# Kernel optimization log

Measured on AMD Instinct MI355X. Metric: run time of the kernel, lower is better.

The kernel has to match this reference:

```python
import jax, jax.numpy as jnp
import numpy as np

# Fuzzy-logic decoder: rules = [[0,0,0],[1,0,1]] (hardcoded in the torch module's __init__).
# For each rule [p, a, b] firing on predicate p:
#   num[s,o] = max_k min(t[a, s, k], t[b, k, o])   (max-min relation composition)
# amalgamate(x, y) = x + y - x*y (probabilistic OR); new starts at 0, and
# amalgamate(x, 0) = x, so with exactly one rule per predicate:
#   t_new[p] = amalgamate(t[p], num_p) = t[p] + num_p - t[p]*num_p

def _compose(A, B):
    # A: [S, K], B: [K, O] -> max over k of elementwise min -> [S, O]
    return jnp.max(jnp.minimum(A[:, :, None], B[None, :, :]), axis=1)


def setup_inputs() -> dict:
    key = jax.random.key(0)
    t = jax.random.uniform(key, (2, 512, 512), dtype=jnp.float32)
    return {"t": t}


def reference(t) -> jnp.ndarray:
    t0, t1 = t[0], t[1]
    num0 = _compose(t0, t0)          # rule [0,0,0]
    num1 = _compose(t0, t1)          # rule [1,0,1]
    num = jnp.stack([num0, num1], axis=0)  # [2, S, O]
    return t + num - t * num         # amalgamate(t, num)
```

## Files before the change

### kernel.cpp

```cpp
#include <hip/hip_runtime.h>


#define SDIM 512
#define TS 64
#define TO 32
#define BK 64
#define BK2 32
#define NCH (SDIM / BK)
#define ASTR 36

typedef _Float16 h2 __attribute__((ext_vector_type(2)));

__device__ __forceinline__ h2 pack2(float a, float b) {
    return __builtin_bit_cast(h2, __builtin_amdgcn_cvt_pkrtz(a, b));
}
__device__ __forceinline__ h2 pmin(h2 a, h2 b) { return __builtin_elementwise_min(a, b); }
__device__ __forceinline__ h2 pmax(h2 a, h2 b) { return __builtin_elementwise_max(a, b); }

__global__ __launch_bounds__(256) void fuzzy_compose_kernel(
        const float* __restrict__ t, float* __restrict__ out) {
    __shared__ h2 Als[TS][ASTR];
    __shared__ h2 Bls[BK2][TO];

    const int tid = threadIdx.x;
    const int o0 = blockIdx.x * TO;
    const int s0 = blockIdx.y * TS;
    const int p  = blockIdx.z;

    const float* __restrict__ A = t;
    const float* __restrict__ B = t + p * (SDIM * SDIM);

    const int og = tid & 15, sg = tid >> 4;
    const int ol = og * 2, sl = sg * 4;

    const int ar = tid >> 2, aq = tid & 3;
    const int bk = tid >> 3, bq = tid & 7;

    const float4* __restrict__ Arow =
        reinterpret_cast<const float4*>(A + (s0 + ar) * SDIM);

    h2 acc[4][2];
    #pragma unroll
    for (int j = 0; j < 4; ++j)
        #pragma unroll
        for (int i = 0; i < 2; ++i)
            acc[j][i] = pack2(0.f, 0.f);

    float4 fa[4], fx, fy;
    #pragma unroll
    for (int q4 = 0; q4 < 4; ++q4) fa[q4] = Arow[aq * 4 + q4];
    fx = *reinterpret_cast<const float4*>(B + (2 * bk) * SDIM + o0 + bq * 4);
    fy = *reinterpret_cast<const float4*>(B + (2 * bk + 1) * SDIM + o0 + bq * 4);

    for (int c = 0; c < NCH; ++c) {
        #pragma unroll
        for (int q4 = 0; q4 < 4; ++q4) {
            Als[ar][aq * 8 + q4 * 2 + 0] = pack2(fa[q4].x, fa[q4].y);
            Als[ar][aq * 8 + q4 * 2 + 1] = pack2(fa[q4].z, fa[q4].w);
        }
        Bls[bk][bq * 4 + 0] = pack2(fx.x, fy.x);
        Bls[bk][bq * 4 + 1] = pack2(fx.y, fy.y);
        Bls[bk][bq * 4 + 2] = pack2(fx.z, fy.z);
        Bls[bk][bq * 4 + 3] = pack2(fx.w, fy.w);
        __syncthreads();

        if (c + 1 < NCH) {
            const int k0 = (c + 1) * BK;
            #pragma unroll
            for (int q4 = 0; q4 < 4; ++q4) fa[q4] = Arow[k0 / 4 + aq * 4 + q4];
            fx = *reinterpret_cast<const float4*>(B + (k0 + 2 * bk) * SDIM + o0 + bq * 4);
            fy = *reinterpret_cast<const float4*>(B + (k0 + 2 * bk + 1) * SDIM + o0 + bq * 4);
        }

        #pragma unroll
        for (int k2 = 0; k2 < BK2; ++k2) {
            const h2 b0 = Bls[k2][ol];
            const h2 b1 = Bls[k2][ol + 1];
            #pragma unroll
            for (int j = 0; j < 4; ++j) {
                const h2 a = Als[sl + j][k2];
                acc[j][0] = pmax(acc[j][0], pmin(a, b0));
                acc[j][1] = pmax(acc[j][1], pmin(a, b1));
            }
        }
        __syncthreads();
    }

    const float* __restrict__ tp = t + p * (SDIM * SDIM);
    float* __restrict__ op = out + p * (SDIM * SDIM);
    #pragma unroll
    for (int j = 0; j < 4; ++j) {
        const int row = s0 + sl + j;
        const float2 tv = *reinterpret_cast<const float2*>(tp + row * SDIM + o0 + ol);
        const float n0 = fmaxf((float)acc[j][0][0], (float)acc[j][0][1]);
        const float n1 = fmaxf((float)acc[j][1][0], (float)acc[j][1][1]);
        float2 r;
        r.x = tv.x + n0 - tv.x * n0;
        r.y = tv.y + n1 - tv.y * n1;
        *reinterpret_cast<float2*>(op + row * SDIM + o0 + ol) = r;
    }
}

extern "C" void kernel_launch(void* const* d_in, const int* in_sizes, int n_in,
                              void* d_out, int out_size, void* d_ws, size_t ws_size,
                              hipStream_t stream) {
    const float* t = (const float*)d_in[0];
    float* out = (float*)d_out;
    dim3 grid(SDIM / TO, SDIM / TS, 2);
    fuzzy_compose_kernel<<<grid, 256, 0, stream>>>(t, out);
}
```

Measured before the change: 72.22 us.

## Split K across blocks with fp16 partials and a max-reduce finalize kernel

Measured after the change: 139.0 us. 1.92x slower.

```diff
diff --git a/kernel.cpp b/kernel.cpp
--- a/kernel.cpp
+++ b/kernel.cpp
@@ -4,10 +4,11 @@
 #define SDIM 512
 #define TS 64
 #define TO 32
+#define SPLIT 4
+#define KB 128
 #define BK 64
 #define BK2 32
-#define NCH (SDIM / BK)
-#define ASTR 36
+#define NCH (KB / BK)
 
 typedef _Float16 h2 __attribute__((ext_vector_type(2)));
 
@@ -16,89 +17,117 @@
 }
 __device__ __forceinline__ h2 pmin(h2 a, h2 b) { return __builtin_elementwise_min(a, b); }
 __device__ __forceinline__ h2 pmax(h2 a, h2 b) { return __builtin_elementwise_max(a, b); }
+__device__ __forceinline__ h2 bch2(unsigned u) { return __builtin_bit_cast(h2, u); }
 
-__global__ __launch_bounds__(256) void fuzzy_compose_kernel(
-        const float* __restrict__ t, float* __restrict__ out) {
-    __shared__ h2 Als[TS][ASTR];
+__global__ __launch_bounds__(256, 4) void compose_part(
+        const float* __restrict__ t, _Float16* __restrict__ part) {
+    __shared__ h2 AlsT[BK2][TS];
     __shared__ h2 Bls[BK2][TO];
 
     const int tid = threadIdx.x;
     const int o0 = blockIdx.x * TO;
     const int s0 = blockIdx.y * TS;
-    const int p  = blockIdx.z;
+    const int p  = blockIdx.z >> 2;
+    const int sp = blockIdx.z & 3;
+    const int kbase = sp * KB;
 
-    const float* __restrict__ A = t;
     const float* __restrict__ B = t + p * (SDIM * SDIM);
 
-    const int og = tid & 15, sg = tid >> 4;
-    const int ol = og * 2, sl = sg * 4;
-
+    const int ol = (tid & 15) * 2, sl = (tid >> 4) * 4;
     const int ar = tid >> 2, aq = tid & 3;
     const int bk = tid >> 3, bq = tid & 7;
 
     const float4* __restrict__ Arow =
-        reinterpret_cast<const float4*>(A + (s0 + ar) * SDIM);
+        reinterpret_cast<const float4*>(t + (s0 + ar) * SDIM + kbase);
 
     h2 acc[4][2];
     #pragma unroll
-    for (int j = 0; j < 4; ++j)
-        #pragma unroll
-        for (int i = 0; i < 2; ++i)
-            acc[j][i] = pack2(0.f, 0.f);
+    for (int j = 0; j < 4; ++j) {
+        acc[j][0] = pack2(0.f, 0.f);
+        acc[j][1] = pack2(0.f, 0.f);
+    }
 
     float4 fa[4], fx, fy;
     #pragma unroll
     for (int q4 = 0; q4 < 4; ++q4) fa[q4] = Arow[aq * 4 + q4];
-    fx = *reinterpret_cast<const float4*>(B + (2 * bk) * SDIM + o0 + bq * 4);
-    fy = *reinterpret_cast<const float4*>(B + (2 * bk + 1) * SDIM + o0 + bq * 4);
+    fx = *reinterpret_cast<const float4*>(B + (kbase + 2 * bk) * SDIM + o0 + bq * 4);
+    fy = *reinterpret_cast<const float4*>(B + (kbase + 2 * bk + 1) * SDIM + o0 + bq * 4);
 
+    #pragma unroll
     for (int c = 0; c < NCH; ++c) {
         #pragma unroll
         for (int q4 = 0; q4 < 4; ++q4) {
-            Als[ar][aq * 8 + q4 * 2 + 0] = pack2(fa[q4].x, fa[q4].y);
-            Als[ar][aq * 8 + q4 * 2 + 1] = pack2(fa[q4].z, fa[q4].w);
+            const int k2 = aq * 8 + q4 * 2;
+            AlsT[k2 + 0][ar] = pack2(fa[q4].x, fa[q4].y);
+            AlsT[k2 + 1][ar] = pack2(fa[q4].z, fa[q4].w);
         }
-        Bls[bk][bq * 4 + 0] = pack2(fx.x, fy.x);
-        Bls[bk][bq * 4 + 1] = pack2(fx.y, fy.y);
-        Bls[bk][bq * 4 + 2] = pack2(fx.z, fy.z);
-        Bls[bk][bq * 4 + 3] = pack2(fx.w, fy.w);
+        {
+            h2 b0 = pack2(fx.x, fy.x), b1 = pack2(fx.y, fy.y);
+            h2 b2 = pack2(fx.z, fy.z), b3 = pack2(fx.w, fy.w);
+            uint4 u;
+            u.x = __builtin_bit_cast(unsigned, b0);
+            u.y = __builtin_bit_cast(unsigned, b1);
+            u.z = __builtin_bit_cast(unsigned, b2);
+            u.w = __builtin_bit_cast(unsigned, b3);
+            *reinterpret_cast<uint4*>(&Bls[bk][bq * 4]) = u;
+        }
         __syncthreads();
 
         if (c + 1 < NCH) {
             const int k0 = (c + 1) * BK;
             #pragma unroll
             for (int q4 = 0; q4 < 4; ++q4) fa[q4] = Arow[k0 / 4 + aq * 4 + q4];
-            fx = *reinterpret_cast<const float4*>(B + (k0 + 2 * bk) * SDIM + o0 + bq * 4);
-            fy = *reinterpret_cast<const float4*>(B + (k0 + 2 * bk + 1) * SDIM + o0 + bq * 4);
+            fx = *reinterpret_cast<const float4*>(B + (kbase + k0 + 2 * bk) * SDIM + o0 + bq * 4);
+            fy = *reinterpret_cast<const float4*>(B + (kbase + k0 + 2 * bk + 1) * SDIM + o0 + bq * 4);
         }
 
         #pragma unroll
         for (int k2 = 0; k2 < BK2; ++k2) {
-            const h2 b0 = Bls[k2][ol];
-            const h2 b1 = Bls[k2][ol + 1];
-            #pragma unroll
-            for (int j = 0; j < 4; ++j) {
-                const h2 a = Als[sl + j][k2];
-                acc[j][0] = pmax(acc[j][0], pmin(a, b0));
-                acc[j][1] = pmax(acc[j][1], pmin(a, b1));
-            }
+            const uint4 ua = *reinterpret_cast<const uint4*>(&AlsT[k2][sl]);
+            const uint2 ub = *reinterpret_cast<const uint2*>(&Bls[k2][ol]);
+            const h2 b0 = bch2(ub.x), b1 = bch2(ub.y);
+            const h2 a0 = bch2(ua.x), a1 = bch2(ua.y), a2 = bch2(ua.z), a3 = bch2(ua.w);
+            acc[0][0] = pmax(acc[0][0], pmin(a0, b0));
+            acc[0][1] = pmax(acc[0][1], pmin(a0, b1));
+            acc[1][0] = pmax(acc[1][0], pmin(a1, b0));
+            acc[1][1] = pmax(acc[1][1], pmin(a1, b1));
+            acc[2][0] = pmax(acc[2][0], pmin(a2, b0));
+            acc[2][1] = pmax(acc[2][1], pmin(a2, b1));
+            acc[3][0] = pmax(acc[3][0], pmin(a3, b0));
+            acc[3][1] = pmax(acc[3][1], pmin(a3, b1));
         }
         __syncthreads();
     }
 
-    const float* __restrict__ tp = t + p * (SDIM * SDIM);
-    float* __restrict__ op = out + p * (SDIM * SDIM);
     #pragma unroll
     for (int j = 0; j < 4; ++j) {
-        const int row = s0 + sl + j;
-        const float2 tv = *reinterpret_cast<const float2*>(tp + row * SDIM + o0 + ol);
         const float n0 = fmaxf((float)acc[j][0][0], (float)acc[j][0][1]);
         const float n1 = fmaxf((float)acc[j][1][0], (float)acc[j][1][1]);
-        float2 r;
-        r.x = tv.x + n0 - tv.x * n0;
-        r.y = tv.y + n1 - tv.y * n1;
-        *reinterpret_cast<float2*>(op + row * SDIM + o0 + ol) = r;
+        const h2 pr = pack2(n0, n1);
+        const int idx = ((p * SPLIT + sp) * SDIM + (s0 + sl + j)) * SDIM + o0 + ol;
+        *reinterpret_cast<h2*>(part + idx) = pr;
     }
+}
+
+__global__ __launch_bounds__(256) void finalize_kernel(
+        const float* __restrict__ t, const _Float16* __restrict__ part,
+        float* __restrict__ out) {
+    const int i2 = blockIdx.x * 256 + threadIdx.x;
+    const h2* __restrict__ ph = reinterpret_cast<const h2*>(part);
+    const int ps = i2 >> 8;
+    const int c2 = i2 & 255;
+    const int p = ps >> 9, s = ps & 511;
+    const int base = (p * SPLIT) * (SDIM * SDIM / 2) + s * (SDIM / 2) + c2;
+    h2 m = ph[base];
+    m = pmax(m, ph[base + 1 * (SDIM * SDIM / 2)]);
+    m = pmax(m, ph[base + 2 * (SDIM * SDIM / 2)]);
+    m = pmax(m, ph[base + 3 * (SDIM * SDIM / 2)]);
+    const float2 tv = reinterpret_cast<const float2*>(t)[i2];
+    const float n0 = (float)m[0], n1 = (float)m[1];
+    float2 r;
+    r.x = tv.x + n0 - tv.x * n0;
+    r.y = tv.y + n1 - tv.y * n1;
+    reinterpret_cast<float2*>(out)[i2] = r;
 }
 
 extern "C" void kernel_launch(void* const* d_in, const int* in_sizes, int n_in,
@@ -106,6 +135,11 @@
                               hipStream_t stream) {
     const float* t = (const float*)d_in[0];
     float* out = (float*)d_out;
-    dim3 grid(SDIM / TO, SDIM / TS, 2);
-    fuzzy_compose_kernel<<<grid, 256, 0, stream>>>(t, out);
+    _Float16* part = (_Float16*)d_ws;
+
+    dim3 grid1(SDIM / TO, SDIM / TS, 2 * SPLIT);
+    compose_part<<<grid1, 256, 0, stream>>>(t, part);
+
+    const int n2 = 2 * SDIM * SDIM / 2;
+    finalize_kernel<<<n2 / 256, 256, 0, stream>>>(t, part, out);
 }
```

## Halve row tile, transpose and swizzle A in LDS, vectorize LDS reads

Applied to the files above, without the earlier changes.

New measurement: 69.55 us. 1.04x faster.

```diff
diff --git a/kernel.cpp b/kernel.cpp
--- a/kernel.cpp
+++ b/kernel.cpp
@@ -2,12 +2,12 @@
 
 
 #define SDIM 512
-#define TS 64
+#define TS 32
 #define TO 32
 #define BK 64
 #define BK2 32
 #define NCH (SDIM / BK)
-#define ASTR 36
+#define BSTR 36
 
 typedef _Float16 h2 __attribute__((ext_vector_type(2)));
 
@@ -16,72 +16,73 @@
 }
 __device__ __forceinline__ h2 pmin(h2 a, h2 b) { return __builtin_elementwise_min(a, b); }
 __device__ __forceinline__ h2 pmax(h2 a, h2 b) { return __builtin_elementwise_max(a, b); }
+__device__ __forceinline__ h2 bch2(unsigned u) { return __builtin_bit_cast(h2, u); }
 
-__global__ __launch_bounds__(256) void fuzzy_compose_kernel(
+__global__ __launch_bounds__(256, 2) void fuzzy_compose_kernel(
         const float* __restrict__ t, float* __restrict__ out) {
-    __shared__ h2 Als[TS][ASTR];
-    __shared__ h2 Bls[BK2][TO];
+    __shared__ h2 AlsT[BK2][TS];
+    __shared__ h2 Bls[BK2][BSTR];
 
     const int tid = threadIdx.x;
     const int o0 = blockIdx.x * TO;
     const int s0 = blockIdx.y * TS;
     const int p  = blockIdx.z;
 
-    const float* __restrict__ A = t;
     const float* __restrict__ B = t + p * (SDIM * SDIM);
 
-    const int og = tid & 15, sg = tid >> 4;
-    const int ol = og * 2, sl = sg * 4;
-
-    const int ar = tid >> 2, aq = tid & 3;
-    const int bk = tid >> 3, bq = tid & 7;
+    const int ol = (tid & 15) * 2, sl = (tid >> 4) * 2;
+    const int ar = tid >> 3, aq = tid & 7;
+    const int acol = ar ^ (aq << 2);
+    const int bk2 = tid >> 3, bq = tid & 7;
 
     const float4* __restrict__ Arow =
-        reinterpret_cast<const float4*>(A + (s0 + ar) * SDIM);
+        reinterpret_cast<const float4*>(t + (s0 + ar) * SDIM);
 
-    h2 acc[4][2];
-    #pragma unroll
-    for (int j = 0; j < 4; ++j)
-        #pragma unroll
-        for (int i = 0; i < 2; ++i)
-            acc[j][i] = pack2(0.f, 0.f);
+    h2 acc[2][2];
+    acc[0][0] = pack2(0.f, 0.f); acc[0][1] = pack2(0.f, 0.f);
+    acc[1][0] = pack2(0.f, 0.f); acc[1][1] = pack2(0.f, 0.f);
 
-    float4 fa[4], fx, fy;
-    #pragma unroll
-    for (int q4 = 0; q4 < 4; ++q4) fa[q4] = Arow[aq * 4 + q4];
-    fx = *reinterpret_cast<const float4*>(B + (2 * bk) * SDIM + o0 + bq * 4);
-    fy = *reinterpret_cast<const float4*>(B + (2 * bk + 1) * SDIM + o0 + bq * 4);
+    float4 fa0, fa1, fx, fy;
+    fa0 = Arow[aq * 2 + 0];
+    fa1 = Arow[aq * 2 + 1];
+    fx = *reinterpret_cast<const float4*>(B + (2 * bk2) * SDIM + o0 + bq * 4);
+    fy = *reinterpret_cast<const float4*>(B + (2 * bk2 + 1) * SDIM + o0 + bq * 4);
 
     for (int c = 0; c < NCH; ++c) {
-        #pragma unroll
-        for (int q4 = 0; q4 < 4; ++q4) {
-            Als[ar][aq * 8 + q4 * 2 + 0] = pack2(fa[q4].x, fa[q4].y);
-            Als[ar][aq * 8 + q4 * 2 + 1] = pack2(fa[q4].z, fa[q4].w);
+        {
+            const int k2b = aq * 4;
+            AlsT[k2b + 0][acol] = pack2(fa0.x, fa0.y);
+            AlsT[k2b + 1][acol] = pack2(fa0.z, fa0.w);
+            AlsT[k2b + 2][acol] = pack2(fa1.x, fa1.y);
+            AlsT[k2b + 3][acol] = pack2(fa1.z, fa1.w);
+            uint4 u;
+            u.x = __builtin_bit_cast(unsigned, pack2(fx.x, fy.x));
+            u.y = __builtin_bit_cast(unsigned, pack2(fx.y, fy.y));
+            u.z = __builtin_bit_cast(unsigned, pack2(fx.z, fy.z));
+            u.w = __builtin_bit_cast(unsigned, pack2(fx.w, fy.w));
+            *reinterpret_cast<uint4*>(&Bls[bk2][bq * 4]) = u;
         }
-        Bls[bk][bq * 4 + 0] = pack2(fx.x, fy.x);
-        Bls[bk][bq * 4 + 1] = pack2(fx.y, fy.y);
-        Bls[bk][bq * 4 + 2] = pack2(fx.z, fy.z);
-        Bls[bk][bq * 4 + 3] = pack2(fx.w, fy.w);
         __syncthreads();
 
         if (c + 1 < NCH) {
             const int k0 = (c + 1) * BK;
-            #pragma unroll
-            for (int q4 = 0; q4 < 4; ++q4) fa[q4] = Arow[k0 / 4 + aq * 4 + q4];
-            fx = *reinterpret_cast<const float4*>(B + (k0 + 2 * bk) * SDIM + o0 + bq * 4);
-            fy = *reinterpret_cast<const float4*>(B + (k0 + 2 * bk + 1) * SDIM + o0 + bq * 4);
+            fa0 = Arow[k0 / 4 + aq * 2 + 0];
+            fa1 = Arow[k0 / 4 + aq * 2 + 1];
+            fx = *reinterpret_cast<const float4*>(B + (k0 + 2 * bk2) * SDIM + o0 + bq * 4);
+            fy = *reinterpret_cast<const float4*>(B + (k0 + 2 * bk2 + 1) * SDIM + o0 + bq * 4);
         }
 
         #pragma unroll
         for (int k2 = 0; k2 < BK2; ++k2) {
-            const h2 b0 = Bls[k2][ol];
-            const h2 b1 = Bls[k2][ol + 1];
-            #pragma unroll
-            for (int j = 0; j < 4; ++j) {
-                const h2 a = Als[sl + j][k2];
-                acc[j][0] = pmax(acc[j][0], pmin(a, b0));
-                acc[j][1] = pmax(acc[j][1], pmin(a, b1));
-            }
+            const int swz = ((k2 >> 2) & 7) << 2;
+            const uint2 ua = *reinterpret_cast<const uint2*>(&AlsT[k2][sl ^ swz]);
+            const uint2 ub = *reinterpret_cast<const uint2*>(&Bls[k2][ol]);
+            const h2 a0 = bch2(ua.x), a1 = bch2(ua.y);
+            const h2 b0 = bch2(ub.x), b1 = bch2(ub.y);
+            acc[0][0] = pmax(acc[0][0], pmin(a0, b0));
+            acc[0][1] = pmax(acc[0][1], pmin(a0, b1));
+            acc[1][0] = pmax(acc[1][0], pmin(a1, b0));
+            acc[1][1] = pmax(acc[1][1], pmin(a1, b1));
         }
         __syncthreads();
     }
@@ -89,7 +90,7 @@
     const float* __restrict__ tp = t + p * (SDIM * SDIM);
     float* __restrict__ op = out + p * (SDIM * SDIM);
     #pragma unroll
-    for (int j = 0; j < 4; ++j) {
+    for (int j = 0; j < 2; ++j) {
         const int row = s0 + sl + j;
         const float2 tv = *reinterpret_cast<const float2*>(tp + row * SDIM + o0 + ol);
         const float n0 = fmaxf((float)acc[j][0][0], (float)acc[j][0][1]);
```

## Double-buffer LDS tiles with transposed swizzled A and vectorized shared loads

Applied to the files above, without the earlier changes.

New measurement: 141.5 us. 95.9% more time.

```diff
diff --git a/kernel.cpp b/kernel.cpp
--- a/kernel.cpp
+++ b/kernel.cpp
@@ -4,10 +4,10 @@
 #define SDIM 512
 #define TS 64
 #define TO 32
-#define BK 64
-#define BK2 32
-#define NCH (SDIM / BK)
-#define ASTR 36
+#define BK 128
+#define BK2 64
+#define NCH 4
+#define BSTR 36
 
 typedef _Float16 h2 __attribute__((ext_vector_type(2)));
 
@@ -16,74 +16,108 @@
 }
 __device__ __forceinline__ h2 pmin(h2 a, h2 b) { return __builtin_elementwise_min(a, b); }
 __device__ __forceinline__ h2 pmax(h2 a, h2 b) { return __builtin_elementwise_max(a, b); }
+__device__ __forceinline__ h2 bch2(unsigned u) { return __builtin_bit_cast(h2, u); }
+__device__ __forceinline__ unsigned b32(h2 v) { return __builtin_bit_cast(unsigned, v); }
 
-__global__ __launch_bounds__(256) void fuzzy_compose_kernel(
+__global__ __launch_bounds__(256, 2) void fuzzy_compose_kernel(
         const float* __restrict__ t, float* __restrict__ out) {
-    __shared__ h2 Als[TS][ASTR];
-    __shared__ h2 Bls[BK2][TO];
+    __shared__ h2 AlsT[2][BK2][TS];
+    __shared__ h2 Bls[2][BK2][BSTR];
 
     const int tid = threadIdx.x;
     const int o0 = blockIdx.x * TO;
     const int s0 = blockIdx.y * TS;
     const int p  = blockIdx.z;
+    const float* __restrict__ Bmat = t + p * (SDIM * SDIM);
 
-    const float* __restrict__ A = t;
-    const float* __restrict__ B = t + p * (SDIM * SDIM);
-
-    const int og = tid & 15, sg = tid >> 4;
-    const int ol = og * 2, sl = sg * 4;
+    const int ol = (tid & 15) * 2;
+    const int sl = (tid >> 4) * 4;
 
     const int ar = tid >> 2, aq = tid & 3;
-    const int bk = tid >> 3, bq = tid & 7;
+    const int acol = ar ^ (aq << 3);
+    const int bk2 = tid >> 3, bq = tid & 7;
 
     const float4* __restrict__ Arow =
-        reinterpret_cast<const float4*>(A + (s0 + ar) * SDIM);
+        reinterpret_cast<const float4*>(t + (s0 + ar) * SDIM);
 
     h2 acc[4][2];
     #pragma unroll
-    for (int j = 0; j < 4; ++j)
-        #pragma unroll
-        for (int i = 0; i < 2; ++i)
-            acc[j][i] = pack2(0.f, 0.f);
+    for (int j = 0; j < 4; ++j) {
+        acc[j][0] = pack2(0.f, 0.f);
+        acc[j][1] = pack2(0.f, 0.f);
+    }
 
-    float4 fa[4], fx, fy;
+    float4 fa[8], fb[4];
+
     #pragma unroll
-    for (int q4 = 0; q4 < 4; ++q4) fa[q4] = Arow[aq * 4 + q4];
-    fx = *reinterpret_cast<const float4*>(B + (2 * bk) * SDIM + o0 + bq * 4);
-    fy = *reinterpret_cast<const float4*>(B + (2 * bk + 1) * SDIM + o0 + bq * 4);
+    for (int q = 0; q < 8; ++q) fa[q] = Arow[aq + 4 * q];
+    #pragma unroll
+    for (int r = 0; r < 4; ++r)
+        fb[r] = *reinterpret_cast<const float4*>(Bmat + (4 * bk2 + r) * SDIM + o0 + bq * 4);
+
+    #pragma unroll
+    for (int q = 0; q < 8; ++q) {
+        const int k2 = (aq + 4 * q) * 2;
+        AlsT[0][k2 + 0][acol] = pack2(fa[q].x, fa[q].y);
+        AlsT[0][k2 + 1][acol] = pack2(fa[q].z, fa[q].w);
+    }
+    {
+        uint4 u0, u1;
+        u0.x = b32(pack2(fb[0].x, fb[1].x)); u0.y = b32(pack2(fb[0].y, fb[1].y));
+        u0.z = b32(pack2(fb[0].z, fb[1].z)); u0.w = b32(pack2(fb[0].w, fb[1].w));
+        u1.x = b32(pack2(fb[2].x, fb[3].x)); u1.y = b32(pack2(fb[2].y, fb[3].y));
+        u1.z = b32(pack2(fb[2].z, fb[3].z)); u1.w = b32(pack2(fb[2].w, fb[3].w));
+        *reinterpret_cast<uint4*>(&Bls[0][2 * bk2 + 0][bq * 4]) = u0;
+        *reinterpret_cast<uint4*>(&Bls[0][2 * bk2 + 1][bq * 4]) = u1;
+    }
 
     for (int c = 0; c < NCH; ++c) {
-        #pragma unroll
-        for (int q4 = 0; q4 < 4; ++q4) {
-            Als[ar][aq * 8 + q4 * 2 + 0] = pack2(fa[q4].x, fa[q4].y);
-            Als[ar][aq * 8 + q4 * 2 + 1] = pack2(fa[q4].z, fa[q4].w);
-        }
-        Bls[bk][bq * 4 + 0] = pack2(fx.x, fy.x);
-        Bls[bk][bq * 4 + 1] = pack2(fx.y, fy.y);
-        Bls[bk][bq * 4 + 2] = pack2(fx.z, fy.z);
-        Bls[bk][bq * 4 + 3] = pack2(fx.w, fy.w);
         __syncthreads();
 
         if (c + 1 < NCH) {
-            const int k0 = (c + 1) * BK;
+            const int kf4 = (c + 1) * (BK / 4);
             #pragma unroll
-            for (int q4 = 0; q4 < 4; ++q4) fa[q4] = Arow[k0 / 4 + aq * 4 + q4];
-            fx = *reinterpret_cast<const float4*>(B + (k0 + 2 * bk) * SDIM + o0 + bq * 4);
-            fy = *reinterpret_cast<const float4*>(B + (k0 + 2 * bk + 1) * SDIM + o0 + bq * 4);
+            for (int q = 0; q < 8; ++q) fa[q] = Arow[kf4 + aq + 4 * q];
+            #pragma unroll
+            for (int r = 0; r < 4; ++r)
+                fb[r] = *reinterpret_cast<const float4*>(
+                    Bmat + ((c + 1) * BK + 4 * bk2 + r) * SDIM + o0 + bq * 4);
         }
 
+        const int buf = c & 1;
         #pragma unroll
         for (int k2 = 0; k2 < BK2; ++k2) {
-            const h2 b0 = Bls[k2][ol];
-            const h2 b1 = Bls[k2][ol + 1];
+            const int swz = ((k2 >> 1) & 3) << 3;
+            const uint4 ua = *reinterpret_cast<const uint4*>(&AlsT[buf][k2][sl ^ swz]);
+            const uint2 ub = *reinterpret_cast<const uint2*>(&Bls[buf][k2][ol]);
+            const h2 b0 = bch2(ub.x), b1 = bch2(ub.y);
+            const h2 a0 = bch2(ua.x), a1 = bch2(ua.y), a2 = bch2(ua.z), a3 = bch2(ua.w);
+            acc[0][0] = pmax(acc[0][0], pmin(a0, b0));
+            acc[0][1] = pmax(acc[0][1], pmin(a0, b1));
+            acc[1][0] = pmax(acc[1][0], pmin(a1, b0));
+            acc[1][1] = pmax(acc[1][1], pmin(a1, b1));
+            acc[2][0] = pmax(acc[2][0], pmin(a2, b0));
+            acc[2][1] = pmax(acc[2][1], pmin(a2, b1));
+            acc[3][0] = pmax(acc[3][0], pmin(a3, b0));
+            acc[3][1] = pmax(acc[3][1], pmin(a3, b1));
+        }
+
+        if (c + 1 < NCH) {
+            const int nb = (c + 1) & 1;
             #pragma unroll
-            for (int j = 0; j < 4; ++j) {
-                const h2 a = Als[sl + j][k2];
-                acc[j][0] = pmax(acc[j][0], pmin(a, b0));
-                acc[j][1] = pmax(acc[j][1], pmin(a, b1));
+            for (int q = 0; q < 8; ++q) {
+                const int k2 = (aq + 4 * q) * 2;
+                AlsT[nb][k2 + 0][acol] = pack2(fa[q].x, fa[q].y);
+                AlsT[nb][k2 + 1][acol] = pack2(fa[q].z, fa[q].w);
             }
+            uint4 u0, u1;
+            u0.x = b32(pack2(fb[0].x, fb[1].x)); u0.y = b32(pack2(fb[0].y, fb[1].y));
+            u0.z = b32(pack2(fb[0].z, fb[1].z)); u0.w = b32(pack2(fb[0].w, fb[1].w));
+            u1.x = b32(pack2(fb[2].x, fb[3].x)); u1.y = b32(pack2(fb[2].y, fb[3].y));
+            u1.z = b32(pack2(fb[2].z, fb[3].z)); u1.w = b32(pack2(fb[2].w, fb[3].w));
+            *reinterpret_cast<uint4*>(&Bls[nb][2 * bk2 + 0][bq * 4]) = u0;
+            *reinterpret_cast<uint4*>(&Bls[nb][2 * bk2 + 1][bq * 4]) = u1;
         }
-        __syncthreads();
     }
 
     const float* __restrict__ tp = t + p * (SDIM * SDIM);
```
